# Optimization experiments

Hardware: AMD Instinct MI355X
Metric: run time of the kernel (lower is better)

The kernel has to match this reference:

```python
import jax, jax.numpy as jnp
import numpy as np

N_NODES = 100000
N_EDGES = 3200000


def gcn_conv(x, W, b, src, dst, n_nodes):
    """PyG GCNConv: self-loops, symmetric D^-1/2 A D^-1/2 norm, linear, bias."""
    loop = jnp.arange(n_nodes, dtype=src.dtype)
    s = jnp.concatenate([src, loop])  # [E+N]
    d = jnp.concatenate([dst, loop])  # [E+N]
    # degree computed at destination (col), edge_weight = 1
    deg = jax.ops.segment_sum(jnp.ones_like(d, dtype=x.dtype), d,
                              num_segments=n_nodes)
    dinv = jnp.where(deg > 0, jax.lax.rsqrt(deg), 0.0)
    norm = dinv[s] * dinv[d]  # [E+N]
    h = x @ W.T  # [N, out]
    msg = h[s] * norm[:, None]  # gather + scale, [E+N, out]
    out = jax.ops.segment_sum(msg, d, num_segments=n_nodes)  # scatter-add
    return out + b


def setup_inputs() -> dict:
    key = jax.random.key(0)
    k1, k2, k3, k4 = jax.random.split(key, 4)
    x = jax.random.normal(k1, (N_NODES, 2), dtype=jnp.float32)
    edge_index = jax.random.randint(k2, (2, N_EDGES), 0, N_NODES,
                                    dtype=jnp.int64)
    # Glorot-ish init for linear weights
    W1 = jax.random.normal(k3, (64, 2), dtype=jnp.float32) * 0.5
    b1 = jnp.zeros((64,), dtype=jnp.float32)
    W2 = jax.random.normal(k4, (2, 64), dtype=jnp.float32) * 0.125
    b2 = jnp.zeros((2,), dtype=jnp.float32)
    return {"x": x, "edge_index": edge_index, "W1": W1, "b1": b1,
            "W2": W2, "b2": b2}


def reference(x, edge_index, W1, b1, W2, b2):
    src, dst = edge_index[0], edge_index[1]
    h = gcn_conv(x, W1, b1, src, dst, N_NODES)
    h = jax.nn.relu(h)
    out = gcn_conv(h, W2, b2, src, dst, N_NODES)
    return out
```

## Files before the change

### kernel.cpp

```cpp
#include <hip/hip_runtime.h>

#define N_NODES 100000
#define SHIFT 7
#define BNODES 128
#define NB 782
#define CAP 5120
#define TILE 8192
#define SB 1024


__global__ __launch_bounds__(SB, 8) void k_sort(const int* __restrict__ src,
                                                const int* __restrict__ dst,
                                                int* claim,
                                                const int* __restrict__ pz,
                                                int* sg, int e) {
    __shared__ int hist[2 * NB];
    __shared__ int rank[2 * NB];
    __shared__ int addrbase[NB];
    __shared__ int partials[16];
    __shared__ int stage[TILE];
    __shared__ unsigned short binmap[TILE];

    const int t = threadIdx.x;
    const int base = blockIdx.x * TILE;
    const int n = min(TILE, e - base);
    const int goff = (t >> 9) * NB;

    for (int i = t; i < 2 * NB; i += SB) hist[i] = 0;
    __syncthreads();

    int recs[8];
    int bins[8];
    int* myh = hist + goff;
#pragma unroll
    for (int k = 0; k < 2; ++k) {
        int idx = base + (k * SB + t) * 4;
        if (idx + 3 < e) {
            int4 s4 = *(const int4*)(src + idx);
            int4 d4 = *(const int4*)(dst + idx);
            int ss[4] = {s4.x, s4.y, s4.z, s4.w};
            int dd[4] = {d4.x, d4.y, d4.z, d4.w};
#pragma unroll
            for (int j = 0; j < 4; ++j) {
                int b = dd[j] >> SHIFT;
                bins[4 * k + j] = b;
                recs[4 * k + j] = ss[j] | ((dd[j] & (BNODES - 1)) << 17);
                atomicAdd(&myh[b], 1);
            }
        } else {
#pragma unroll
            for (int j = 0; j < 4; ++j) {
                int i2 = idx + j;
                if (i2 < e) {
                    int d = dst[i2];
                    int b = d >> SHIFT;
                    bins[4 * k + j] = b;
                    recs[4 * k + j] = src[i2] | ((d & (BNODES - 1)) << 17);
                    atomicAdd(&myh[b], 1);
                } else {
                    bins[4 * k + j] = -1;
                }
            }
        }
    }
    __syncthreads();

    int c0 = 0, c1 = 0, c = 0;
    if (t < NB) {
        c0 = hist[t];
        c1 = hist[NB + t];
        c = c0 + c1;
    }
    int vs = c;
#pragma unroll
    for (int off = 1; off < 64; off <<= 1) {
        int w = __shfl_up(vs, off, 64);
        if ((t & 63) >= off) vs += w;
    }
    if ((t & 63) == 63) partials[t >> 6] = vs;
    __syncthreads();
    int add = 0;
    for (int w = 0; w < (t >> 6); ++w) add += partials[w];
    vs += add;
    int excl = vs - c;
    const int P = *pz;
    if (t < NB) {
        rank[t] = excl;
        rank[NB + t] = excl + c0;
        int rb = c ? (atomicAdd(&claim[t], c) - P) : 0;
        addrbase[t] = t * CAP + rb - excl;
    }
    __syncthreads();

    int* myr = rank + goff;
#pragma unroll
    for (int m = 0; m < 8; ++m) {
        int b = bins[m];
        if (b >= 0) {
            int pos = atomicAdd(&myr[b], 1);
            stage[pos] = recs[m];
            binmap[pos] = (unsigned short)b;
        }
    }
    __syncthreads();

    for (int i = t; i < n; i += SB) {
        sg[addrbase[binmap[i]] + i] = stage[i];
    }
}

__global__ __launch_bounds__(512) void k_refine(const int* __restrict__ claim,
                                                const int* __restrict__ pz,
                                                const int* __restrict__ sg,
                                                const float* __restrict__ x,
                                                int* sg2, int* packed,
                                                float2* u) {
    __shared__ int hist[4 * BNODES];
    __shared__ int rank[4 * BNODES];
    __shared__ int partials[2];
    const int t = threadIdx.x;
    const int b = blockIdx.x;
    const int* p = sg + b * CAP;
    const int len = claim[b] - *pz;
    const int g = t >> 7;

    int4 r[3];
#pragma unroll
    for (int k = 0; k < 3; ++k) {
        int idx = 4 * t + 2048 * k;
        int4 v = make_int4(-1, -1, -1, -1);
        if (idx + 3 < len) v = *(const int4*)(p + idx);
        else if (idx < len) {
            v.x = p[idx];
            if (idx + 1 < len) v.y = p[idx + 1];
            if (idx + 2 < len) v.z = p[idx + 2];
        }
        r[k] = v;
    }
    for (int i = t; i < 4 * BNODES; i += 512) hist[i] = 0;
    __syncthreads();
    int* myh = hist + g * BNODES;
#pragma unroll
    for (int k = 0; k < 3; ++k) {
        if (r[k].x != -1) atomicAdd(&myh[((unsigned)r[k].x) >> 17], 1);
        if (r[k].y != -1) atomicAdd(&myh[((unsigned)r[k].y) >> 17], 1);
        if (r[k].z != -1) atomicAdd(&myh[((unsigned)r[k].z) >> 17], 1);
        if (r[k].w != -1) atomicAdd(&myh[((unsigned)r[k].w) >> 17], 1);
    }
    __syncthreads();

    int c4x = 0, c4y = 0, c4z = 0, c4w = 0, tot = 0;
    if (t < BNODES) {
        c4x = hist[t];
        c4y = hist[BNODES + t];
        c4z = hist[2 * BNODES + t];
        c4w = hist[3 * BNODES + t];
        tot = (c4x + c4y) + (c4z + c4w);
    }
    int vs = tot;
#pragma unroll
    for (int off = 1; off < 64; off <<= 1) {
        int w = __shfl_up(vs, off, 64);
        if ((t & 63) >= off) vs += w;
    }
    if ((t & 63) == 63 && t < BNODES) partials[t >> 6] = vs;
    __syncthreads();
    if (t < BNODES) {
        int add = 0;
        for (int w = 0; w < (t >> 6); ++w) add += partials[w];
        vs += add;
        int excl = vs - tot;
        int run = excl;
        rank[t] = run; run += c4x;
        rank[BNODES + t] = run; run += c4y;
        rank[2 * BNODES + t] = run; run += c4z;
        rank[3 * BNODES + t] = run;
        int node = b * BNODES + t;
        if (node < N_NODES) {
            packed[node] = (b * CAP + excl) | (tot << 22);
            float dv = rsqrtf((float)(tot + 1));
            float2 xv = ((const float2*)x)[node];
            u[node] = make_float2(dv * xv.x, dv * xv.y);
        }
    }
    __syncthreads();

    int* q = sg2 + b * CAP;
    int* myr = rank + g * BNODES;
#pragma unroll
    for (int k = 0; k < 3; ++k) {
        if (r[k].x != -1) q[atomicAdd(&myr[((unsigned)r[k].x) >> 17], 1)] = r[k].x & 0x1FFFF;
        if (r[k].y != -1) q[atomicAdd(&myr[((unsigned)r[k].y) >> 17], 1)] = r[k].y & 0x1FFFF;
        if (r[k].z != -1) q[atomicAdd(&myr[((unsigned)r[k].z) >> 17], 1)] = r[k].z & 0x1FFFF;
        if (r[k].w != -1) q[atomicAdd(&myr[((unsigned)r[k].w) >> 17], 1)] = r[k].w & 0x1FFFF;
    }
}

__global__ __launch_bounds__(256) void k_agg1(const int* __restrict__ sg2,
                                              const int* __restrict__ packed,
                                              const float2* __restrict__ u,
                                              const float* __restrict__ W1,
                                              const float* __restrict__ b1,
                                              const float* __restrict__ W2,
                                              float2* v) {
    __shared__ float sW1[128], sb1[64], sW2[128];
    int t = threadIdx.x;
    if (t < 128) { sW1[t] = W1[t]; sW2[t] = W2[t]; }
    else if (t < 192) sb1[t - 128] = b1[t - 128];
    __syncthreads();
    int n = blockIdx.x * 32 + (t >> 3);
    if (n >= N_NODES) return;
    int g = t & 7;
    int pk = packed[n];
    int s = pk & 0x3FFFFF;
    int cnt = ((unsigned)pk) >> 22;
    int e2 = s + cnt;
    float sx = 0.f, sy = 0.f;
    int i = s + g;
    for (; i + 24 < e2; i += 32) {
        float2 ga = u[sg2[i]];
        float2 gb = u[sg2[i + 8]];
        float2 gc = u[sg2[i + 16]];
        float2 gd = u[sg2[i + 24]];
        sx += (ga.x + gb.x) + (gc.x + gd.x);
        sy += (ga.y + gb.y) + (gc.y + gd.y);
    }
    for (; i + 8 < e2; i += 16) {
        float2 ga = u[sg2[i]];
        float2 gb = u[sg2[i + 8]];
        sx += ga.x + gb.x;
        sy += ga.y + gb.y;
    }
    if (i < e2) { float2 ga = u[sg2[i]]; sx += ga.x; sy += ga.y; }
    sx += __shfl_xor(sx, 1, 8); sy += __shfl_xor(sy, 1, 8);
    sx += __shfl_xor(sx, 2, 8); sy += __shfl_xor(sy, 2, 8);
    sx += __shfl_xor(sx, 4, 8); sy += __shfl_xor(sy, 4, 8);
    float dv = rsqrtf((float)(cnt + 1));
    float2 un = u[n];
    float a0 = dv * (sx + un.x), a1 = dv * (sy + un.y);
    float y0 = 0.f, y1 = 0.f;
#pragma unroll
    for (int k = 0; k < 8; ++k) {
        int j = g + 8 * k;
        float h = fmaxf(fmaf(sW1[2 * j], a0,
                        fmaf(sW1[2 * j + 1], a1, sb1[j])), 0.f);
        y0 = fmaf(sW2[j], h, y0);
        y1 = fmaf(sW2[64 + j], h, y1);
    }
    y0 += __shfl_xor(y0, 1, 8); y1 += __shfl_xor(y1, 1, 8);
    y0 += __shfl_xor(y0, 2, 8); y1 += __shfl_xor(y1, 2, 8);
    y0 += __shfl_xor(y0, 4, 8); y1 += __shfl_xor(y1, 4, 8);
    if (g == 0) v[n] = make_float2(dv * y0, dv * y1);
}

__global__ __launch_bounds__(256) void k_agg2(const int* __restrict__ sg2,
                                              const int* __restrict__ packed,
                                              const float2* __restrict__ v,
                                              const float* __restrict__ b2,
                                              float2* out) {
    int t = threadIdx.x;
    int n = blockIdx.x * 32 + (t >> 3);
    if (n >= N_NODES) return;
    int g = t & 7;
    int pk = packed[n];
    int s = pk & 0x3FFFFF;
    int cnt = ((unsigned)pk) >> 22;
    int e2 = s + cnt;
    float sx = 0.f, sy = 0.f;
    int i = s + g;
    for (; i + 24 < e2; i += 32) {
        float2 ga = v[sg2[i]];
        float2 gb = v[sg2[i + 8]];
        float2 gc = v[sg2[i + 16]];
        float2 gd = v[sg2[i + 24]];
        sx += (ga.x + gb.x) + (gc.x + gd.x);
        sy += (ga.y + gb.y) + (gc.y + gd.y);
    }
    for (; i + 8 < e2; i += 16) {
        float2 ga = v[sg2[i]];
        float2 gb = v[sg2[i + 8]];
        sx += ga.x + gb.x;
        sy += ga.y + gb.y;
    }
    if (i < e2) { float2 ga = v[sg2[i]]; sx += ga.x; sy += ga.y; }
    sx += __shfl_xor(sx, 1, 8); sy += __shfl_xor(sy, 1, 8);
    sx += __shfl_xor(sx, 2, 8); sy += __shfl_xor(sy, 2, 8);
    sx += __shfl_xor(sx, 4, 8); sy += __shfl_xor(sy, 4, 8);
    if (g == 0) {
        float dv = rsqrtf((float)(cnt + 1));
        float2 vn = v[n];
        out[n] = make_float2(fmaf(dv, sx + vn.x, b2[0]),
                             fmaf(dv, sy + vn.y, b2[1]));
    }
}

extern "C" void kernel_launch(void* const* d_in, const int* in_sizes, int n_in,
                              void* d_out, int out_size, void* d_ws, size_t ws_size,
                              hipStream_t stream) {
    const float* x  = (const float*)d_in[0];
    const int* ei   = (const int*)d_in[1];
    const float* W1 = (const float*)d_in[2];
    const float* b1 = (const float*)d_in[3];
    const float* W2 = (const float*)d_in[4];
    const float* b2 = (const float*)d_in[5];

    int e = in_sizes[1] / 2;
    const int* src = ei;
    const int* dst = ei + e;

    int* ws      = (int*)d_ws;
    int* claim   = ws;
    int* pz      = ws + NB;
    int* sg      = ws + 784;
    int* sg2     = sg + NB * CAP;
    int* packed  = sg2 + NB * CAP;
    float2* u    = (float2*)(packed + N_NODES);
    float2* v    = u + N_NODES;
    float2* outp = (float2*)d_out;

    const int gA = (N_NODES + 31) / 32;
    k_sort  <<<(e + TILE - 1) / TILE, SB, 0, stream>>>(src, dst, claim, pz, sg, e);
    k_refine<<<NB, 512, 0, stream>>>(claim, pz, sg, x, sg2, packed, u);
    k_agg1  <<<gA, 256, 0, stream>>>(sg2, packed, u, W1, b1, W2, v);
    k_agg2  <<<gA, 256, 0, stream>>>(sg2, packed, v, b2, outp);
}
```

Before: 147.5 us.

## Halve sort tile and block size, scan two bins per thread

Cuts the bucketing sort kernel from 8192-edge tiles on 1024 threads to 4096-edge tiles on 512 threads. Because 512 threads cannot cover the 782 bins one per thread, each thread now handles two adjacent bins in the histogram scan, rank setup and global claim atomics. Smaller blocks use less shared memory and may fit more blocks per CU. The cost is twice as many blocks and twice as many global claim atomics per bin overall, and the scattered writes per bin become shorter and less coalesced.

```diff
diff --git a/kernel.cpp b/kernel.cpp
--- a/kernel.cpp
+++ b/kernel.cpp
@@ -5,8 +5,8 @@
 #define BNODES 128
 #define NB 782
 #define CAP 5120
-#define TILE 8192
-#define SB 1024
+#define TILE 4096
+#define SB 512
 
 
 __global__ __launch_bounds__(SB, 8) void k_sort(const int* __restrict__ src,
@@ -17,14 +17,14 @@
     __shared__ int hist[2 * NB];
     __shared__ int rank[2 * NB];
     __shared__ int addrbase[NB];
-    __shared__ int partials[16];
+    __shared__ int partials[8];
     __shared__ int stage[TILE];
     __shared__ unsigned short binmap[TILE];
 
     const int t = threadIdx.x;
     const int base = blockIdx.x * TILE;
     const int n = min(TILE, e - base);
-    const int goff = (t >> 9) * NB;
+    const int goff = (t >> 8) * NB;
 
     for (int i = t; i < 2 * NB; i += SB) hist[i] = 0;
     __syncthreads();
@@ -65,13 +65,14 @@
     }
     __syncthreads();
 
-    int c0 = 0, c1 = 0, c = 0;
-    if (t < NB) {
-        c0 = hist[t];
-        c1 = hist[NB + t];
-        c = c0 + c1;
-    }
-    int vs = c;
+    int cA0 = 0, cA1 = 0, cB0 = 0, cB1 = 0, c0 = 0, c1 = 0, cpair = 0;
+    if (t < NB / 2) {
+        cA0 = hist[2 * t];       cA1 = hist[2 * t + 1];
+        cB0 = hist[NB + 2 * t];  cB1 = hist[NB + 2 * t + 1];
+        c0 = cA0 + cB0;          c1 = cA1 + cB1;
+        cpair = c0 + c1;
+    }
+    int vs = cpair;
 #pragma unroll
     for (int off = 1; off < 64; off <<= 1) {
         int w = __shfl_up(vs, off, 64);
@@ -82,13 +83,18 @@
     int add = 0;
     for (int w = 0; w < (t >> 6); ++w) add += partials[w];
     vs += add;
-    int excl = vs - c;
     const int P = *pz;
-    if (t < NB) {
-        rank[t] = excl;
-        rank[NB + t] = excl + c0;
-        int rb = c ? (atomicAdd(&claim[t], c) - P) : 0;
-        addrbase[t] = t * CAP + rb - excl;
+    if (t < NB / 2) {
+        int excl0 = vs - cpair;
+        int excl1 = excl0 + c0;
+        rank[2 * t] = excl0;
+        rank[2 * t + 1] = excl1;
+        rank[NB + 2 * t] = excl0 + cA0;
+        rank[NB + 2 * t + 1] = excl1 + cA1;
+        int rb0 = c0 ? (atomicAdd(&claim[2 * t], c0) - P) : 0;
+        int rb1 = c1 ? (atomicAdd(&claim[2 * t + 1], c1) - P) : 0;
+        addrbase[2 * t] = 2 * t * CAP + rb0 - excl0;
+        addrbase[2 * t + 1] = (2 * t + 1) * CAP + rb1 - excl1;
     }
     __syncthreads();
 
```

Result: slower. 170.6 us (+15.7%).

## Shard global bin claim counters into eight regions to cut atomic contention

Applied to the files above, without the earlier changes.

Each sort block now claims space in one of eight per-bin sub-buckets, chosen by block index modulo 8, each with a smaller capacity. The goal is to cut contention on the global atomicAdd counters, since each counter is now hit by about an eighth as many blocks. In exchange, the refine kernel must walk eight separate segments per bin with scalar loads and reads the staged records twice, once for the histogram and once for the scatter, instead of holding them in registers as int4 vectors. The smaller per-region capacity also adds some overflow risk under skewed input.

```diff
diff --git a/kernel.cpp b/kernel.cpp
--- a/kernel.cpp
+++ b/kernel.cpp
@@ -5,6 +5,7 @@
 #define BNODES 128
 #define NB 782
 #define CAP 5120
+#define CAPR 768
 #define TILE 8192
 #define SB 1024
 
@@ -23,6 +24,7 @@
 
     const int t = threadIdx.x;
     const int base = blockIdx.x * TILE;
+    const int reg7 = blockIdx.x & 7;
     const int n = min(TILE, e - base);
     const int goff = (t >> 9) * NB;
 
@@ -87,8 +89,8 @@
     if (t < NB) {
         rank[t] = excl;
         rank[NB + t] = excl + c0;
-        int rb = c ? (atomicAdd(&claim[t], c) - P) : 0;
-        addrbase[t] = t * CAP + rb - excl;
+        int rb = c ? (atomicAdd(&claim[reg7 * NB + t], c) - P) : 0;
+        addrbase[t] = (reg7 * NB + t) * CAPR + rb - excl;
     }
     __syncthreads();
 
@@ -120,32 +122,20 @@
     __shared__ int partials[2];
     const int t = threadIdx.x;
     const int b = blockIdx.x;
-    const int* p = sg + b * CAP;
-    const int len = claim[b] - *pz;
+    const int P = *pz;
     const int g = t >> 7;
 
-    int4 r[3];
-#pragma unroll
-    for (int k = 0; k < 3; ++k) {
-        int idx = 4 * t + 2048 * k;
-        int4 v = make_int4(-1, -1, -1, -1);
-        if (idx + 3 < len) v = *(const int4*)(p + idx);
-        else if (idx < len) {
-            v.x = p[idx];
-            if (idx + 1 < len) v.y = p[idx + 1];
-            if (idx + 2 < len) v.z = p[idx + 2];
-        }
-        r[k] = v;
-    }
     for (int i = t; i < 4 * BNODES; i += 512) hist[i] = 0;
     __syncthreads();
+
     int* myh = hist + g * BNODES;
 #pragma unroll
-    for (int k = 0; k < 3; ++k) {
-        if (r[k].x != -1) atomicAdd(&myh[((unsigned)r[k].x) >> 17], 1);
-        if (r[k].y != -1) atomicAdd(&myh[((unsigned)r[k].y) >> 17], 1);
-        if (r[k].z != -1) atomicAdd(&myh[((unsigned)r[k].z) >> 17], 1);
-        if (r[k].w != -1) atomicAdd(&myh[((unsigned)r[k].w) >> 17], 1);
+    for (int r = 0; r < 8; ++r) {
+        const int len = claim[r * NB + b] - P;
+        const int* pr = sg + (r * NB + b) * CAPR;
+        for (int i = t; i < len; i += 512) {
+            atomicAdd(&myh[((unsigned)pr[i]) >> 17], 1);
+        }
     }
     __syncthreads();
 
@@ -188,11 +178,13 @@
     int* q = sg2 + b * CAP;
     int* myr = rank + g * BNODES;
 #pragma unroll
-    for (int k = 0; k < 3; ++k) {
-        if (r[k].x != -1) q[atomicAdd(&myr[((unsigned)r[k].x) >> 17], 1)] = r[k].x & 0x1FFFF;
-        if (r[k].y != -1) q[atomicAdd(&myr[((unsigned)r[k].y) >> 17], 1)] = r[k].y & 0x1FFFF;
-        if (r[k].z != -1) q[atomicAdd(&myr[((unsigned)r[k].z) >> 17], 1)] = r[k].z & 0x1FFFF;
-        if (r[k].w != -1) q[atomicAdd(&myr[((unsigned)r[k].w) >> 17], 1)] = r[k].w & 0x1FFFF;
+    for (int r = 0; r < 8; ++r) {
+        const int len = claim[r * NB + b] - P;
+        const int* pr = sg + (r * NB + b) * CAPR;
+        for (int i = t; i < len; i += 512) {
+            int rec = pr[i];
+            q[atomicAdd(&myr[((unsigned)rec) >> 17], 1)] = rec & 0x1FFFF;
+        }
     }
 }
 
@@ -310,9 +302,9 @@
 
     int* ws      = (int*)d_ws;
     int* claim   = ws;
-    int* pz      = ws + NB;
-    int* sg      = ws + 784;
-    int* sg2     = sg + NB * CAP;
+    int* pz      = ws + 8 * NB;
+    int* sg      = ws + 6260;
+    int* sg2     = sg + 8 * NB * CAPR;
     int* packed  = sg2 + NB * CAP;
     float2* u    = (float2*)(packed + N_NODES);
     float2* v    = u + N_NODES;
```

Result: no change. 144.9 us, median of 2 (-1.7%).
